# Optimization experiments

Measured on AMD Instinct MI355X. Metric: run time of the kernel, lower is better.

Reference implementation:

```python
import jax, jax.numpy as jnp
import numpy as np

EPS = 1e-5

def layernorm(x, g, b):
    mu = jnp.mean(x, axis=-1, keepdims=True)
    var = jnp.var(x, axis=-1, keepdims=True)
    return (x - mu) * jax.lax.rsqrt(var + EPS) * g + b

def setup_inputs() -> dict:
    key = jax.random.key(0)
    ks = jax.random.split(key, 12)
    B, S, D, H, F = 2, 2048, 1024, 16, 4096
    sd = 0.02
    x = jax.random.normal(ks[0], (B, S, D), dtype=jnp.float32)
    mask = jnp.tril(jnp.ones((S, S), dtype=jnp.int32))[None, None]  # causal [1,1,S,S]
    return {
        "x": x,
        "mask": mask,
        "ln1_g": jnp.ones((D,), jnp.float32),
        "ln1_b": jnp.zeros((D,), jnp.float32),
        "Wqkv": jax.random.normal(ks[1], (D, 3 * D), jnp.float32) * sd,
        "bqkv": jnp.zeros((3 * D,), jnp.float32),
        "Wo": jax.random.normal(ks[2], (D, D), jnp.float32) * sd,
        "bo": jnp.zeros((D,), jnp.float32),
        "ln2_g": jnp.ones((D,), jnp.float32),
        "ln2_b": jnp.zeros((D,), jnp.float32),
        "W1": jax.random.normal(ks[3], (D, F), jnp.float32) * sd,
        "b1": jnp.zeros((F,), jnp.float32),
        "W2": jax.random.normal(ks[4], (F, D), jnp.float32) * sd,
        "b2": jnp.zeros((D,), jnp.float32),
    }

def reference(x, mask, ln1_g, ln1_b, Wqkv, bqkv, Wo, bo, ln2_g, ln2_b, W1, b1, W2, b2):
    B, S, D = x.shape
    H = 16
    hd = D // H
    scale = hd ** -0.5
    # --- attention sublayer (pre-LN) ---
    h = layernorm(x, ln1_g, ln1_b)
    qkv = h @ Wqkv + bqkv                             # [B,S,3D]
    qkv = qkv.reshape(B, S, 3, H, hd)
    q = jnp.transpose(qkv[:, :, 0], (0, 2, 1, 3))      # [B,H,S,hd]
    k = jnp.transpose(qkv[:, :, 1], (0, 2, 1, 3))
    v = jnp.transpose(qkv[:, :, 2], (0, 2, 1, 3))
    scores = jnp.einsum('bhqd,bhkd->bhqk', q, k) * scale
    scores = jnp.where(mask == 0, -jnp.inf, scores)
    attn = jax.nn.softmax(scores, axis=-1)
    out = jnp.einsum('bhqk,bhkd->bhqd', attn, v)
    out = jnp.transpose(out, (0, 2, 1, 3)).reshape(B, S, D)
    x = x + (out @ Wo + bo)
    # --- FFN sublayer (pre-LN) ---
    h = layernorm(x, ln2_g, ln2_b)
    h = jax.nn.gelu(h @ W1 + b1, approximate=False)
    x = x + (h @ W2 + b2)
    return x
```

## Files before the change

kernel.cpp:

```cpp
#include <hip/hip_runtime.h>

typedef __bf16 bf16x8 __attribute__((ext_vector_type(8)));
typedef float f32x4 __attribute__((ext_vector_type(4)));

typedef const void __attribute__((address_space(1))) gvoid_t;
typedef void __attribute__((address_space(3))) lvoid_t;

__device__ __forceinline__ void gload16(const void* g, void* l) {
  __builtin_amdgcn_global_load_lds((gvoid_t*)g, (lvoid_t*)l, 16, 0, 0);
}

__device__ __forceinline__ unsigned short f2b(float f) {
  unsigned int u = __builtin_bit_cast(unsigned int, f);
  u = (u + 0x7FFFu + ((u >> 16) & 1u)) >> 16;
  return (unsigned short)u;
}

__global__ __launch_bounds__(256) void ln_kernel(
    const float* __restrict__ x, const float* __restrict__ g,
    const float* __restrict__ b, unsigned short* __restrict__ out) {
  const int row = blockIdx.x;
  const int t = threadIdx.x;
  const float4 v = *(const float4*)(x + (size_t)row * 1024 + t * 4);
  float s1 = v.x + v.y + v.z + v.w;
  float s2 = v.x * v.x + v.y * v.y + v.z * v.z + v.w * v.w;
#pragma unroll
  for (int off = 32; off > 0; off >>= 1) {
    s1 += __shfl_down(s1, off, 64);
    s2 += __shfl_down(s2, off, 64);
  }
  __shared__ float red[8];
  const int wid = t >> 6;
  if ((t & 63) == 0) { red[wid] = s1; red[wid + 4] = s2; }
  __syncthreads();
  s1 = red[0] + red[1] + red[2] + red[3];
  s2 = red[4] + red[5] + red[6] + red[7];
  const float mu = s1 * (1.0f / 1024.0f);
  const float var = s2 * (1.0f / 1024.0f) - mu * mu;
  const float rs = rsqrtf(var + 1e-5f);
  const float4 gv = *(const float4*)(g + t * 4);
  const float4 bv = *(const float4*)(b + t * 4);
  ushort4 o;
  o.x = f2b((v.x - mu) * rs * gv.x + bv.x);
  o.y = f2b((v.y - mu) * rs * gv.y + bv.y);
  o.z = f2b((v.z - mu) * rs * gv.z + bv.z);
  o.w = f2b((v.w - mu) * rs * gv.w + bv.w);
  *(ushort4*)(out + (size_t)row * 1024 + t * 4) = o;
}

__global__ __launch_bounds__(256) void convT_kernel(
    const float* __restrict__ W, unsigned short* __restrict__ Wt,
    int K, int N) {
  __shared__ float tl[32][33];
  const int n0 = blockIdx.x * 32, k0 = blockIdx.y * 32;
  const int tx = threadIdx.x & 31, ty = threadIdx.x >> 5;
#pragma unroll
  for (int i = 0; i < 4; ++i) {
    int k = ty + i * 8;
    tl[k][tx] = W[(size_t)(k0 + k) * N + n0 + tx];
  }
  __syncthreads();
#pragma unroll
  for (int i = 0; i < 4; ++i) {
    int n = ty + i * 8;
    Wt[(size_t)(n0 + n) * K + k0 + tx] = f2b(tl[tx][n]);
  }
}

__global__ __launch_bounds__(256) void transv_kernel(
    const unsigned short* __restrict__ qkv, unsigned short* __restrict__ vt) {
  __shared__ unsigned short tl[64][72];
  const int bh = blockIdx.x;
  const int b = bh >> 4, h = bh & 15;
  const int s0 = blockIdx.y * 64;
  const int t = threadIdx.x;
  const int sr = t >> 3, dcol = (t & 7) * 8;
#pragma unroll
  for (int half = 0; half < 2; ++half) {
    const int s = sr + half * 32;
    const uint4 v = *(const uint4*)(qkv + ((size_t)(b * 2048 + s0 + s)) * 3072 + 2048 + h * 64 + dcol);
    *(uint4*)&tl[s][dcol] = v;
  }
  __syncthreads();
  const int d0 = t >> 3, sc = (t & 7) * 8;
#pragma unroll
  for (int half = 0; half < 2; ++half) {
    const int dd = d0 + half * 32;
    alignas(16) unsigned short tmp[8];
#pragma unroll
    for (int j = 0; j < 8; ++j) tmp[j] = tl[sc + j][dd];
    *(uint4*)(vt + ((size_t)bh * 64 + dd) * 2048 + s0 + sc) = *(const uint4*)tmp;
  }
}

template <int EPI>
__global__ __launch_bounds__(256) void gemm_kernel(
    const unsigned short* __restrict__ A, const unsigned short* __restrict__ Bt,
    const float* __restrict__ bias, const float* __restrict__ resid,
    float* __restrict__ Cf, unsigned short* __restrict__ Cb,
    int M, int N, int K) {
  __shared__ __align__(16) char lds[49152];
  const int tid = threadIdx.x;
  const int lane = tid & 63, w = tid >> 6;
  const int wr = w >> 1, wc = w & 1;
  const int bm0 = blockIdx.x * 128, bn0 = blockIdx.y * 128;

  f32x4 acc[4][4] = {};

  const int gcol = (lane & 3) ^ ((lane >> 3) & 3);
  const unsigned short* gA =
      A + (size_t)(bm0 + w * 32 + (lane >> 2)) * K + gcol * 8;
  const unsigned short* gB =
      Bt + (size_t)(bn0 + w * 32 + (lane >> 2)) * K + gcol * 8;
  const size_t rstep = (size_t)16 * K;
  const int woff = w * 2048;

  const int l15 = lane & 15;
  const int g = lane >> 4;

  const int nt = K >> 5;

  auto STAGE = [&](int t, int buf) {
    const int k0 = t << 5;
    char* base = lds + buf * 16384;
    gload16(gA + k0, base + woff);
    gload16(gA + rstep + k0, base + woff + 1024);
    gload16(gB + k0, base + 8192 + woff);
    gload16(gB + rstep + k0, base + 8192 + woff + 1024);
  };

  STAGE(0, 0);
  STAGE(1 < nt ? 1 : 0, 1);
  int cur = 0;

  for (int t = 0; t < nt; ++t) {
    asm volatile("s_waitcnt vmcnt(4)" ::: "memory");
    __builtin_amdgcn_sched_barrier(0);
    __builtin_amdgcn_s_barrier();
    __builtin_amdgcn_sched_barrier(0);

    const char* ldsA = lds + cur * 16384;
    const char* ldsB = ldsA + 8192;
    bf16x8 af[4], bfr[4];
#pragma unroll
    for (int m = 0; m < 4; ++m) {
      const int tr = wr * 64 + m * 16 + l15;
      const int slot = g ^ ((tr >> 1) & 3);
      af[m] = *(const bf16x8*)(ldsA + tr * 64 + slot * 16);
    }
#pragma unroll
    for (int n = 0; n < 4; ++n) {
      const int tc = wc * 64 + n * 16 + l15;
      const int slot = g ^ ((tc >> 1) & 3);
      bfr[n] = *(const bf16x8*)(ldsB + tc * 64 + slot * 16);
    }
#pragma unroll
    for (int m = 0; m < 4; ++m)
#pragma unroll
      for (int n = 0; n < 4; ++n)
        acc[m][n] =
            __builtin_amdgcn_mfma_f32_16x16x32_bf16(af[m], bfr[n], acc[m][n], 0, 0, 0);

    __builtin_amdgcn_sched_barrier(0);
    const int t2 = (t + 2 < nt) ? t + 2 : nt - 1;
    STAGE(t2, cur ? cur - 1 : 2);
    cur = (cur == 2) ? 0 : cur + 1;
  }

#pragma unroll
  for (int mm = 0; mm < 4; ++mm) {
    const int r0 = bm0 + wr * 64 + mm * 16 + (g << 2);
#pragma unroll
    for (int nn = 0; nn < 4; ++nn) {
      const int c = bn0 + wc * 64 + nn * 16 + l15;
      const float bv = bias[c];
#pragma unroll
      for (int i = 0; i < 4; ++i) {
        const size_t idx = (size_t)(r0 + i) * N + c;
        float v = acc[mm][nn][i] + bv;
        if constexpr (EPI == 1) {
          v += resid[idx];
          Cf[idx] = v;
        } else if constexpr (EPI == 2) {
          v = 0.5f * v * (1.0f + erff(v * 0.70710678118654752f));
          Cb[idx] = f2b(v);
        } else if constexpr (EPI == 3) {
          Cb[idx] = f2b(v);
        } else {
          Cf[idx] = v;
        }
      }
    }
  }
}

template <int EPI>
__global__ __launch_bounds__(512) void gemm8w_kernel(
    const unsigned short* __restrict__ A, const unsigned short* __restrict__ Bt,
    const float* __restrict__ bias, const float* __restrict__ resid,
    float* __restrict__ Cf, unsigned short* __restrict__ Cb,
    int M, int N, int K) {
  __shared__ __align__(16) char lds[73728];
  const int tid = threadIdx.x;
  const int lane = tid & 63, w = tid >> 6;
  const int wr = w >> 1, wc = w & 1;
  const int bm0 = blockIdx.x * 256, bn0 = blockIdx.y * 128;

  f32x4 acc[4][4] = {};

  const int gcol = (lane & 3) ^ ((lane >> 3) & 3);
  const unsigned short* gA =
      A + (size_t)(bm0 + w * 32 + (lane >> 2)) * K + gcol * 8;
  const unsigned short* gB =
      Bt + (size_t)(bn0 + w * 16 + (lane >> 2)) * K + gcol * 8;
  const size_t rstep = (size_t)16 * K;

  const int l15 = lane & 15;
  const int g = lane >> 4;

  const int nt = K >> 5;

  auto STAGE = [&](int t, int buf) {
    const int k0 = t << 5;
    char* base = lds + buf * 24576;
    gload16(gA + k0, base + w * 2048);
    gload16(gA + rstep + k0, base + w * 2048 + 1024);
    gload16(gB + k0, base + 16384 + w * 1024);
  };

  STAGE(0, 0);
  STAGE(1 < nt ? 1 : 0, 1);
  int cur = 0;

  for (int t = 0; t < nt; ++t) {
    asm volatile("s_waitcnt vmcnt(3)" ::: "memory");
    __builtin_amdgcn_sched_barrier(0);
    __builtin_amdgcn_s_barrier();
    __builtin_amdgcn_sched_barrier(0);

    const char* ldsA = lds + cur * 24576;
    const char* ldsB = ldsA + 16384;
    bf16x8 af[4], bfr[4];
#pragma unroll
    for (int m = 0; m < 4; ++m) {
      const int tr = wr * 64 + m * 16 + l15;
      const int slot = g ^ ((tr >> 1) & 3);
      af[m] = *(const bf16x8*)(ldsA + tr * 64 + slot * 16);
    }
#pragma unroll
    for (int n = 0; n < 4; ++n) {
      const int tc = wc * 64 + n * 16 + l15;
      const int slot = g ^ ((tc >> 1) & 3);
      bfr[n] = *(const bf16x8*)(ldsB + tc * 64 + slot * 16);
    }
    __builtin_amdgcn_s_setprio(1);
#pragma unroll
    for (int m = 0; m < 4; ++m)
#pragma unroll
      for (int n = 0; n < 4; ++n)
        acc[m][n] =
            __builtin_amdgcn_mfma_f32_16x16x32_bf16(af[m], bfr[n], acc[m][n], 0, 0, 0);
    __builtin_amdgcn_s_setprio(0);

    __builtin_amdgcn_sched_barrier(0);
    const int t2 = (t + 2 < nt) ? t + 2 : nt - 1;
    STAGE(t2, cur ? cur - 1 : 2);
    cur = (cur == 2) ? 0 : cur + 1;
  }

#pragma unroll
  for (int mm = 0; mm < 4; ++mm) {
    const int r0 = bm0 + wr * 64 + mm * 16 + (g << 2);
#pragma unroll
    for (int nn = 0; nn < 4; ++nn) {
      const int c = bn0 + wc * 64 + nn * 16 + l15;
      const float bv = bias[c];
#pragma unroll
      for (int i = 0; i < 4; ++i) {
        const size_t idx = (size_t)(r0 + i) * N + c;
        float v = acc[mm][nn][i] + bv;
        if constexpr (EPI == 1) {
          v += resid[idx];
          Cf[idx] = v;
        } else if constexpr (EPI == 2) {
          v = 0.5f * v * (1.0f + erff(v * 0.70710678118654752f));
          Cb[idx] = f2b(v);
        } else if constexpr (EPI == 3) {
          Cb[idx] = f2b(v);
        } else {
          Cf[idx] = v;
        }
      }
    }
  }
}

__global__ __launch_bounds__(256) void attn_mfma_kernel(
    const unsigned short* __restrict__ qkv, const unsigned short* __restrict__ vt,
    unsigned short* __restrict__ out) {
  __shared__ __align__(16) char Kl[24576];
  __shared__ __align__(16) char Vl[24576];
  __shared__ __align__(16) char Pl[8192];
  const int bh = blockIdx.x;
  const int b = bh >> 4, h = bh & 15;
  const int qtile = (int)gridDim.y - 1 - (int)blockIdx.y;
  const int q0 = qtile * 64;
  const int tid = threadIdx.x;
  const int lane = tid & 63, w = tid >> 6;
  const int l15 = lane & 15, g = lane >> 4;
  const size_t rowbase = (size_t)b * 2048;

  bf16x8 aq[2];
  {
    const unsigned short* qp = qkv + (rowbase + q0 + w * 16 + l15) * 3072 + h * 64 + g * 8;
    aq[0] = __builtin_bit_cast(bf16x8, *(const uint4*)qp);
    aq[1] = __builtin_bit_cast(bf16x8, *(const uint4*)(qp + 32));
  }

  f32x4 oacc[4] = {};
  float mrow[4] = {-1e30f, -1e30f, -1e30f, -1e30f};
  float lrow[4] = {0.f, 0.f, 0.f, 0.f};

  const int srow = w * 16 + (lane >> 3);
  const int slog = (lane & 7) ^ (srow & 7);
  const unsigned short* kS = qkv + (rowbase + srow) * 3072 + 1024 + h * 64 + slog * 8;
  const unsigned short* vS = vt + ((size_t)bh * 64 + srow) * 2048 + slog * 8;
  const int nt = qtile + 1;

  auto STAGE = [&](int t, int buf) {
    const int kb = t * 64;
    char* kd = Kl + buf * 8192 + w * 2048;
    char* vd = Vl + buf * 8192 + w * 2048;
    gload16(kS + (size_t)kb * 3072, kd);
    gload16(kS + (size_t)(kb + 8) * 3072, kd + 1024);
    gload16(vS + kb, vd);
    gload16(vS + kb + 8 * 2048, vd + 1024);
  };

  STAGE(0, 0);
  STAGE(nt > 1 ? 1 : 0, 1);
  int cur = 0;

  for (int kt = 0; kt < nt; ++kt) {
    asm volatile("s_waitcnt vmcnt(4)" ::: "memory");
    __builtin_amdgcn_sched_barrier(0);
    __builtin_amdgcn_s_barrier();
    __builtin_amdgcn_sched_barrier(0);

    const char* Kc = Kl + cur * 8192;
    const char* Vc = Vl + cur * 8192;

    f32x4 sacc[4] = {};
#pragma unroll
    for (int kk = 0; kk < 2; ++kk) {
#pragma unroll
      for (int n = 0; n < 4; ++n) {
        const int r = n * 16 + l15;
        bf16x8 bk = *(const bf16x8*)(Kc + r * 128 + (((kk * 4 + g) ^ (r & 7)) << 4));
        sacc[n] = __builtin_amdgcn_mfma_f32_16x16x32_bf16(aq[kk], bk, sacc[n], 0, 0, 0);
      }
    }

    const bool diag = (kt == qtile);
    float p[4][4];
#pragma unroll
    for (int i = 0; i < 4; ++i) {
      const int qloc = w * 16 + g * 4 + i;
      float sv[4];
      float rm = -1e30f;
#pragma unroll
      for (int n = 0; n < 4; ++n) {
        float s = sacc[n][i] * 0.125f;
        if (diag && (l15 + 16 * n > qloc)) s = -1e30f;
        sv[n] = s;
        rm = fmaxf(rm, s);
      }
#pragma unroll
      for (int off = 8; off >= 1; off >>= 1) rm = fmaxf(rm, __shfl_xor(rm, off, 64));
      const float mnew = fmaxf(mrow[i], rm);
      const float corr = __expf(mrow[i] - mnew);
      mrow[i] = mnew;
      float ls = 0.f;
#pragma unroll
      for (int n = 0; n < 4; ++n) {
        const float pv = __expf(sv[n] - mnew);
        p[n][i] = pv;
        ls += pv;
      }
      lrow[i] = lrow[i] * corr + ls;
#pragma unroll
      for (int dn = 0; dn < 4; ++dn) oacc[dn][i] *= corr;
    }

#pragma unroll
    for (int i = 0; i < 4; ++i) {
      const int r = g * 4 + i;
#pragma unroll
      for (int n = 0; n < 4; ++n) {
        const int col = l15 + 16 * n;
        *(unsigned short*)(Pl + w * 2048 + ((r * 128 + col * 2) ^ ((r & 7) << 4))) = f2b(p[n][i]);
      }
    }
#pragma unroll
    for (int kk = 0; kk < 2; ++kk) {
      bf16x8 ap = *(const bf16x8*)(Pl + w * 2048 + ((l15 * 128 + g * 16 + kk * 64) ^ ((l15 & 7) << 4)));
#pragma unroll
      for (int dn = 0; dn < 4; ++dn) {
        const int r = dn * 16 + l15;
        bf16x8 bv = *(const bf16x8*)(Vc + r * 128 + (((kk * 4 + g) ^ (r & 7)) << 4));
        oacc[dn] = __builtin_amdgcn_mfma_f32_16x16x32_bf16(ap, bv, oacc[dn], 0, 0, 0);
      }
    }

    __builtin_amdgcn_sched_barrier(0);
    const int t2 = (kt + 2 < nt) ? kt + 2 : nt - 1;
    STAGE(t2, cur ? cur - 1 : 2);
    cur = (cur == 2) ? 0 : cur + 1;
  }

#pragma unroll
  for (int i = 0; i < 4; ++i) {
    float l = lrow[i];
#pragma unroll
    for (int off = 8; off >= 1; off >>= 1) l += __shfl_xor(l, off, 64);
    const float inv = 1.0f / l;
    unsigned short* op = out + (rowbase + q0 + w * 16 + g * 4 + i) * 1024 + h * 64 + l15;
#pragma unroll
    for (int dn = 0; dn < 4; ++dn) op[dn * 16] = f2b(oacc[dn][i] * inv);
  }
}

extern "C" void kernel_launch(void* const* d_in, const int* in_sizes, int n_in,
                              void* d_out, int out_size, void* d_ws, size_t ws_size,
                              hipStream_t stream) {
  const float* x = (const float*)d_in[0];
  const float* ln1_g = (const float*)d_in[2];
  const float* ln1_b = (const float*)d_in[3];
  const float* Wqkv = (const float*)d_in[4];
  const float* bqkv = (const float*)d_in[5];
  const float* Wo = (const float*)d_in[6];
  const float* bo = (const float*)d_in[7];
  const float* ln2_g = (const float*)d_in[8];
  const float* ln2_b = (const float*)d_in[9];
  const float* W1 = (const float*)d_in[10];
  const float* b1 = (const float*)d_in[11];
  const float* W2 = (const float*)d_in[12];
  const float* b2 = (const float*)d_in[13];
  float* outp = (float*)d_out;

  const int M = 4096, D = 1024, F = 4096;
  char* ws = (char*)d_ws;
  size_t o = 0;
  auto alloc = [&](size_t bytes) {
    size_t r = o;
    o += (bytes + 255) & ~(size_t)255;
    return r;
  };
  unsigned short* bWqkv = (unsigned short*)(ws + alloc((size_t)3072 * D * 2));
  unsigned short* bWo   = (unsigned short*)(ws + alloc((size_t)D * D * 2));
  unsigned short* bW1   = (unsigned short*)(ws + alloc((size_t)F * D * 2));
  unsigned short* bW2   = (unsigned short*)(ws + alloc((size_t)D * F * 2));
  unsigned short* h     = (unsigned short*)(ws + alloc((size_t)M * D * 2));
  unsigned short* qkvb  = (unsigned short*)(ws + alloc((size_t)M * F * 2));
  unsigned short* attn  = (unsigned short*)(ws + alloc((size_t)M * D * 2));
  float* x1             = (float*)(ws + alloc((size_t)M * D * 4));
  unsigned short* vt    = (unsigned short*)(ws + alloc((size_t)32 * 64 * 2048 * 2));
  unsigned short* f1 = qkvb;
  unsigned short* h2 = h;

  convT_kernel<<<dim3(3072 / 32, D / 32), 256, 0, stream>>>(Wqkv, bWqkv, D, 3072);
  convT_kernel<<<dim3(D / 32, D / 32), 256, 0, stream>>>(Wo, bWo, D, D);
  convT_kernel<<<dim3(F / 32, D / 32), 256, 0, stream>>>(W1, bW1, D, F);
  convT_kernel<<<dim3(D / 32, F / 32), 256, 0, stream>>>(W2, bW2, F, D);

  ln_kernel<<<M, 256, 0, stream>>>(x, ln1_g, ln1_b, h);
  gemm8w_kernel<3><<<dim3(M / 256, 3072 / 128), 512, 0, stream>>>(
      h, bWqkv, bqkv, nullptr, nullptr, qkvb, M, 3072, D);
  transv_kernel<<<dim3(32, 32), 256, 0, stream>>>(qkvb, vt);
  attn_mfma_kernel<<<dim3(32, 32), 256, 0, stream>>>(qkvb, vt, attn);
  gemm_kernel<1><<<dim3(M / 128, D / 128), 256, 0, stream>>>(
      attn, bWo, bo, x, x1, nullptr, M, D, D);
  ln_kernel<<<M, 256, 0, stream>>>(x1, ln2_g, ln2_b, h2);
  gemm8w_kernel<2><<<dim3(M / 256, F / 128), 512, 0, stream>>>(
      h2, bW1, b1, nullptr, nullptr, f1, M, F, D);
  gemm_kernel<1><<<dim3(M / 128, D / 128), 256, 0, stream>>>(
      f1, bW2, b2, x1, outp, nullptr, M, D, F);
}
```

Before: 242.6 us.

## Deepen GEMM K-tile to 64 with 8-way XOR swizzle and add MFMA setprio

The GEMM main loop now stages 64-wide K tiles instead of 32, doubling LDS to 96KB across three buffers. It uses a new 128-byte row layout with an 8-slot XOR swizzle and processes two k-substeps per barrier. This halves the number of barriers and loop iterations per K, at the cost of more LDS per block, which may lower occupancy. Separately, s_setprio raises wave priority around MFMA bursts in both the GEMM and attention kernels, to favour matrix issue over other waves.

```diff
diff --git a/kernel.cpp b/kernel.cpp
--- a/kernel.cpp
+++ b/kernel.cpp
@@ -99,7 +99,7 @@
     const float* __restrict__ bias, const float* __restrict__ resid,
     float* __restrict__ Cf, unsigned short* __restrict__ Cb,
     int M, int N, int K) {
-  __shared__ __align__(16) char lds[49152];
+  __shared__ __align__(16) char lds[98304];
   const int tid = threadIdx.x;
   const int lane = tid & 63, w = tid >> 6;
   const int wr = w >> 1, wc = w & 1;
@@ -107,26 +107,26 @@
 
   f32x4 acc[4][4] = {};
 
-  const int gcol = (lane & 3) ^ ((lane >> 3) & 3);
-  const unsigned short* gA =
-      A + (size_t)(bm0 + w * 32 + (lane >> 2)) * K + gcol * 8;
-  const unsigned short* gB =
-      Bt + (size_t)(bn0 + w * 32 + (lane >> 2)) * K + gcol * 8;
-  const size_t rstep = (size_t)16 * K;
-  const int woff = w * 2048;
+  const int rr = lane >> 3;
+  const int slog = (lane & 7) ^ rr;
+  const unsigned short* gA = A + (size_t)(bm0 + w * 32 + rr) * K + slog * 8;
+  const unsigned short* gB = Bt + (size_t)(bn0 + w * 32 + rr) * K + slog * 8;
+  const size_t rstep8 = (size_t)8 * K;
 
   const int l15 = lane & 15;
   const int g = lane >> 4;
 
-  const int nt = K >> 5;
+  const int nt = K >> 6;
 
   auto STAGE = [&](int t, int buf) {
-    const int k0 = t << 5;
-    char* base = lds + buf * 16384;
-    gload16(gA + k0, base + woff);
-    gload16(gA + rstep + k0, base + woff + 1024);
-    gload16(gB + k0, base + 8192 + woff);
-    gload16(gB + rstep + k0, base + 8192 + woff + 1024);
+    const int k0 = t << 6;
+    char* ab = lds + buf * 32768 + w * 4096;
+    char* bb = lds + buf * 32768 + 16384 + w * 4096;
+#pragma unroll
+    for (int j = 0; j < 4; ++j) {
+      gload16(gA + j * rstep8 + k0, ab + j * 1024);
+      gload16(gB + j * rstep8 + k0, bb + j * 1024);
+    }
   };
 
   STAGE(0, 0);
@@ -134,32 +134,35 @@
   int cur = 0;
 
   for (int t = 0; t < nt; ++t) {
-    asm volatile("s_waitcnt vmcnt(4)" ::: "memory");
+    asm volatile("s_waitcnt vmcnt(8)" ::: "memory");
     __builtin_amdgcn_sched_barrier(0);
     __builtin_amdgcn_s_barrier();
     __builtin_amdgcn_sched_barrier(0);
 
-    const char* ldsA = lds + cur * 16384;
-    const char* ldsB = ldsA + 8192;
-    bf16x8 af[4], bfr[4];
-#pragma unroll
-    for (int m = 0; m < 4; ++m) {
-      const int tr = wr * 64 + m * 16 + l15;
-      const int slot = g ^ ((tr >> 1) & 3);
-      af[m] = *(const bf16x8*)(ldsA + tr * 64 + slot * 16);
-    }
-#pragma unroll
-    for (int n = 0; n < 4; ++n) {
-      const int tc = wc * 64 + n * 16 + l15;
-      const int slot = g ^ ((tc >> 1) & 3);
-      bfr[n] = *(const bf16x8*)(ldsB + tc * 64 + slot * 16);
-    }
-#pragma unroll
-    for (int m = 0; m < 4; ++m)
-#pragma unroll
-      for (int n = 0; n < 4; ++n)
-        acc[m][n] =
-            __builtin_amdgcn_mfma_f32_16x16x32_bf16(af[m], bfr[n], acc[m][n], 0, 0, 0);
+    const char* ldsA = lds + cur * 32768;
+    const char* ldsB = ldsA + 16384;
+#pragma unroll
+    for (int kk = 0; kk < 2; ++kk) {
+      bf16x8 af[4], bfr[4];
+#pragma unroll
+      for (int m = 0; m < 4; ++m) {
+        const int tr = wr * 64 + m * 16 + l15;
+        af[m] = *(const bf16x8*)(ldsA + tr * 128 + (((kk * 4 + g) ^ (tr & 7)) << 4));
+      }
+#pragma unroll
+      for (int n = 0; n < 4; ++n) {
+        const int tc = wc * 64 + n * 16 + l15;
+        bfr[n] = *(const bf16x8*)(ldsB + tc * 128 + (((kk * 4 + g) ^ (tc & 7)) << 4));
+      }
+      __builtin_amdgcn_s_setprio(1);
+#pragma unroll
+      for (int m = 0; m < 4; ++m)
+#pragma unroll
+        for (int n = 0; n < 4; ++n)
+          acc[m][n] =
+              __builtin_amdgcn_mfma_f32_16x16x32_bf16(af[m], bfr[n], acc[m][n], 0, 0, 0);
+      __builtin_amdgcn_s_setprio(0);
+    }
 
     __builtin_amdgcn_sched_barrier(0);
     const int t2 = (t + 2 < nt) ? t + 2 : nt - 1;
@@ -351,6 +354,7 @@
     const char* Vc = Vl + cur * 8192;
 
     f32x4 sacc[4] = {};
+    __builtin_amdgcn_s_setprio(1);
 #pragma unroll
     for (int kk = 0; kk < 2; ++kk) {
 #pragma unroll
@@ -360,6 +364,7 @@
         sacc[n] = __builtin_amdgcn_mfma_f32_16x16x32_bf16(aq[kk], bk, sacc[n], 0, 0, 0);
       }
     }
+    __builtin_amdgcn_s_setprio(0);
 
     const bool diag = (kt == qtile);
     float p[4][4];
@@ -404,12 +409,14 @@
 #pragma unroll
     for (int kk = 0; kk < 2; ++kk) {
       bf16x8 ap = *(const bf16x8*)(Pl + w * 2048 + ((l15 * 128 + g * 16 + kk * 64) ^ ((l15 & 7) << 4)));
+      __builtin_amdgcn_s_setprio(1);
 #pragma unroll
       for (int dn = 0; dn < 4; ++dn) {
         const int r = dn * 16 + l15;
         bf16x8 bv = *(const bf16x8*)(Vc + r * 128 + (((kk * 4 + g) ^ (r & 7)) << 4));
         oacc[dn] = __builtin_amdgcn_mfma_f32_16x16x32_bf16(ap, bv, oacc[dn], 0, 0, 0);
       }
+      __builtin_amdgcn_s_setprio(0);
     }
 
     __builtin_amdgcn_sched_barrier(0);
```

Result: faster. 231.3 us (-4.6%).
